# Optimization experiments

Hardware: AMD Instinct MI355X
Metric: run time of the kernel (lower is better)

Reference implementation:

```python
import jax, jax.numpy as jnp
import numpy as np

D_MODEL = 2048
N_HEADS = 8
EXPAND_K = 1
EXPAND_V = 2
DK = D_MODEL * EXPAND_K // N_HEADS      # 256 per-head key dim
DV = D_MODEL * EXPAND_V // N_HEADS      # 512 per-head value dim
INTER = 5632
EPS = 1e-6
CHUNK = 64


def setup_inputs() -> dict:
    key = jax.random.key(0)
    ks = jax.random.split(key, 12)
    d = D_MODEL
    s = lambda fan_in: 1.0 / np.sqrt(fan_in)
    return {
        "hidden_states": jax.random.normal(ks[0], (2, 2048, d), jnp.float32),
        "attn_norm_w": jnp.ones((d,), jnp.float32),
        "q_w": jax.random.normal(ks[1], (d, d * EXPAND_K), jnp.float32) * s(d),
        "k_w": jax.random.normal(ks[2], (d, d * EXPAND_K), jnp.float32) * s(d),
        "v_w": jax.random.normal(ks[3], (d, d * EXPAND_V), jnp.float32) * s(d),
        "g_w": jax.random.normal(ks[4], (d, d * EXPAND_V), jnp.float32) * s(d),
        "o_w": jax.random.normal(ks[5], (d * EXPAND_V, d), jnp.float32) * s(d * EXPAND_V),
        "gnorm_w": jnp.ones((DV,), jnp.float32),
        "mlp_norm_w": jnp.ones((d,), jnp.float32),
        "gate_w": jax.random.normal(ks[6], (d, INTER * 2), jnp.float32) * s(d),
        "down_w": jax.random.normal(ks[7], (INTER, d), jnp.float32) * s(INTER),
    }


def rmsnorm(x, w, eps=EPS):
    return x * jax.lax.rsqrt(jnp.mean(x * x, axis=-1, keepdims=True) + eps) * w


def rope(x):
    # x: [B, T, H, D]; non-interleaved rotary on full head dim
    T, D = x.shape[1], x.shape[-1]
    inv_freq = 1.0 / (10000.0 ** (jnp.arange(0, D, 2, dtype=jnp.float32) / D))
    ang = jnp.arange(T, dtype=jnp.float32)[:, None] * inv_freq  # [T, D/2]
    cos = jnp.cos(ang)[None, :, None, :]
    sin = jnp.sin(ang)[None, :, None, :]
    x1, x2 = jnp.split(x, 2, axis=-1)
    return jnp.concatenate([x1 * cos - x2 * sin, x2 * cos + x1 * sin], axis=-1)


def chunk_retention(q, k, v):
    # q,k: [B,T,H,Dk], v: [B,T,H,Dv]; chunkwise-recurrent RetNet retention
    B, T, H, Dk = q.shape
    Dv = v.shape[-1]
    C = CHUNK
    N = T // C
    gamma = 1.0 - jnp.exp2(-5.0 - jnp.arange(H, dtype=jnp.float32))  # [H]
    i = jnp.arange(C, dtype=jnp.float32)
    diff = i[:, None] - i[None, :]
    Dmask = jnp.where(diff >= 0, gamma[:, None, None] ** diff, 0.0)   # [H,C,C]
    cross_decay = gamma[:, None] ** (i[None, :] + 1.0)                # [H,C]
    k_decay = gamma[:, None] ** (C - 1.0 - i[None, :])                # [H,C]
    chunk_decay = gamma ** C                                          # [H]

    # -> [N, B, H, C, D]
    to_chunks = lambda x: jnp.moveaxis(
        x.reshape(B, N, C, H, x.shape[-1]).transpose(0, 1, 3, 2, 4), 1, 0)
    qc, kc, vc = to_chunks(q), to_chunks(k), to_chunks(v)

    def body(S, inp):
        qb, kb, vb = inp  # [B,H,C,Dk/Dv]
        attn = jnp.einsum('bhid,bhjd->bhij', qb, kb) * Dmask
        o_intra = jnp.einsum('bhij,bhje->bhie', attn, vb)
        o_cross = jnp.einsum('bhid,bhde->bhie', qb * cross_decay[None, :, :, None], S)
        S = chunk_decay[None, :, None, None] * S + \
            jnp.einsum('bhid,bhie->bhde', kb * k_decay[None, :, :, None], vb)
        return S, o_intra + o_cross

    S0 = jnp.zeros((B, H, Dk, Dv), q.dtype)
    _, o = jax.lax.scan(body, S0, (qc, kc, vc))  # o: [N,B,H,C,Dv]
    return jnp.moveaxis(o, 0, 1).transpose(0, 1, 3, 2, 4).reshape(B, T, H, Dv)


def reference(hidden_states, attn_norm_w, q_w, k_w, v_w, g_w, o_w, gnorm_w,
              mlp_norm_w, gate_w, down_w):
    B, T, d = hidden_states.shape
    residual = hidden_states
    h = rmsnorm(hidden_states, attn_norm_w)

    # MultiScaleRetention
    q = (h @ q_w).reshape(B, T, N_HEADS, DK)
    k = (h @ k_w).reshape(B, T, N_HEADS, DK)
    v = (h @ v_w).reshape(B, T, N_HEADS, DV)
    g = (h @ g_w).reshape(B, T, N_HEADS, DV)
    q, k = rope(q), rope(k)
    q = q * (DK ** -0.5)
    o = chunk_retention(q, k, v)
    # fused RMSNorm + swish gate (per head over Dv)
    o = rmsnorm(o, gnorm_w) * (g * jax.nn.sigmoid(g))
    h = o.reshape(B, T, N_HEADS * DV) @ o_w

    # fused-residual RMSNorm
    residual = h + residual
    h = rmsnorm(residual, mlp_norm_w)

    # SwiGLU MLP
    y = h @ gate_w
    gate, y = jnp.split(y, 2, axis=-1)
    h = (gate * jax.nn.sigmoid(gate) * y) @ down_w
    return residual + h
```

## Files before the change

### kernel.cpp

```cpp
#include <hip/hip_runtime.h>
#include <cstdint>
#include <cstddef>

typedef unsigned short u16;
typedef __attribute__((ext_vector_type(4))) float f32x4;
typedef __attribute__((ext_vector_type(4))) unsigned int u32x4;
typedef __attribute__((ext_vector_type(8))) short s16x8;

__device__ __forceinline__ float b2f(u16 u) {
  union { unsigned int i; float f; } x; x.i = ((unsigned int)u) << 16; return x.f;
}
__device__ __forceinline__ u16 f2b(float f) {
  union { float f; unsigned int i; } x; x.f = f;
  unsigned int i = x.i;
  i += 0x7fffu + ((i >> 16) & 1u);
  return (u16)(i >> 16);
}

__device__ __forceinline__ void mfma_bf16(f32x4& c, u32x4 a, u32x4 b) {
  union { u32x4 u; s16x8 s; } ua, ub;
  ua.u = a; ub.u = b;
  c = __builtin_amdgcn_mfma_f32_16x16x32_bf16(ua.s, ub.s, c, 0, 0, 0);
}

__device__ __forceinline__ void async_ld16(const u16* g, u16* l) {
  typedef __attribute__((address_space(1))) const unsigned int GU;
  typedef __attribute__((address_space(3))) unsigned int LU;
  __builtin_amdgcn_global_load_lds((GU*)g, (LU*)l, 16, 0, 0);
}

__global__ __launch_bounds__(256)
void transpose_cast_kernel(const float* __restrict__ in, u16* __restrict__ out,
                           int K, int N, int ldin) {
  __shared__ float tile[64][65];
  const int nb = N >> 6;
  const int bk = blockIdx.x / nb, bn = blockIdx.x % nb;
  const int k0 = bk * 64, n0 = bn * 64;
  const int tid = threadIdx.x;
#pragma unroll
  for (int p = 0; p < 16; ++p) {
    int idx = p * 256 + tid;
    int r = idx >> 6, c = idx & 63;
    tile[r][c] = in[(size_t)(k0 + r) * ldin + n0 + c];
  }
  __syncthreads();
#pragma unroll
  for (int p = 0; p < 16; ++p) {
    int idx = p * 256 + tid;
    int r = idx >> 6, c = idx & 63;
    out[(size_t)(n0 + r) * K + k0 + c] = f2b(tile[c][r]);
  }
}

__global__ __launch_bounds__(256)
void transpose_k_kernel(const u16* __restrict__ qk, u16* __restrict__ kt) {
  __shared__ u16 tile[64][72];
  const int bid = blockIdx.x;
  const int dd = bid & 3, tt = (bid >> 2) & 31;
  const int h = (bid >> 7) & 7, b = bid >> 10;
  const int t0 = tt * 64, d0 = dd * 64;
  const int tid = threadIdx.x;
#pragma unroll
  for (int p = 0; p < 2; ++p) {
    int idx = p * 256 + tid;
    int r = idx >> 3, cq = (idx & 7) * 8;
    *(uint4*)&tile[r][cq] =
        *(const uint4*)&qk[(size_t)(b * 2048 + t0 + r) * 4096 + 2048 + h * 256 + d0 + cq];
  }
  __syncthreads();
#pragma unroll
  for (int p = 0; p < 2; ++p) {
    int idx = p * 256 + tid;
    int r = idx >> 3, cq = (idx & 7) * 8;
    union { u16 h8[8]; uint4 v4; } o;
#pragma unroll
    for (int j = 0; j < 8; ++j) o.h8[j] = tile[cq + j][r];
    *(uint4*)&kt[((size_t)(b * 8 + h) * 256 + d0 + r) * 2048 + t0 + cq] = o.v4;
  }
}

__global__ __launch_bounds__(256)
void rmsnorm_cast_kernel(const float* __restrict__ x, const float* __restrict__ w,
                         u16* __restrict__ out) {
  const int row = blockIdx.x, tid = threadIdx.x;
  const float* xr = x + (size_t)row * 2048;
  float4 a = ((const float4*)xr)[tid * 2];
  float4 b = ((const float4*)xr)[tid * 2 + 1];
  float ss = a.x*a.x + a.y*a.y + a.z*a.z + a.w*a.w
           + b.x*b.x + b.y*b.y + b.z*b.z + b.w*b.w;
#pragma unroll
  for (int m = 32; m; m >>= 1) ss += __shfl_xor(ss, m);
  __shared__ float ps[4];
  if ((tid & 63) == 0) ps[tid >> 6] = ss;
  __syncthreads();
  const float sc = rsqrtf((ps[0] + ps[1] + ps[2] + ps[3]) * (1.0f / 2048.0f) + 1e-6f);
  const int base = tid * 8;
  const float vals[8] = {a.x, a.y, a.z, a.w, b.x, b.y, b.z, b.w};
  union { u16 h[8]; uint4 v4[2]; } o;
#pragma unroll
  for (int j = 0; j < 8; ++j) o.h[j] = f2b(vals[j] * sc * w[base + j]);
  *(uint4*)&out[(size_t)row * 2048 + base] = o.v4[0];
  *(uint4*)&out[(size_t)row * 2048 + base + 8] = o.v4[1];
}

__global__ __launch_bounds__(256)
void rmsnorm_bf16_kernel(const u16* __restrict__ x, const float* __restrict__ w,
                         u16* __restrict__ out) {
  const int row = blockIdx.x, tid = threadIdx.x;
  union { uint4 v4; u16 h[8]; } p;
  p.v4 = *(const uint4*)&x[(size_t)row * 2048 + tid * 8];
  float v[8];
  float ss = 0.f;
#pragma unroll
  for (int j = 0; j < 8; ++j) { v[j] = b2f(p.h[j]); ss += v[j] * v[j]; }
#pragma unroll
  for (int m = 32; m; m >>= 1) ss += __shfl_xor(ss, m);
  __shared__ float ps[4];
  if ((tid & 63) == 0) ps[tid >> 6] = ss;
  __syncthreads();
  const float sc = rsqrtf((ps[0] + ps[1] + ps[2] + ps[3]) * (1.0f / 2048.0f) + 1e-6f);
  union { u16 h[8]; uint4 v4; } o;
#pragma unroll
  for (int j = 0; j < 8; ++j) o.h[j] = f2b(v[j] * sc * w[tid * 8 + j]);
  *(uint4*)&out[(size_t)row * 2048 + tid * 8] = o.v4;
}

__global__ __launch_bounds__(256)
void rope_table_kernel(float* __restrict__ ct, float* __restrict__ st) {
  const int idx = blockIdx.x * 256 + threadIdx.x;
  const int t = idx >> 7, i = idx & 127;
  const float e = -(float)i * (0.0078125f * log2f(10000.0f));
  const float ang = (float)t * exp2f(e);
  ct[idx] = cosf(ang);
  st[idx] = sinf(ang);
}

__global__ __launch_bounds__(256)
void rope_apply_kernel(u16* __restrict__ x, const float* __restrict__ ct,
                       const float* __restrict__ st, int qoff, float scale) {
  const int gid = blockIdx.x * 256 + threadIdx.x;
  const int r = gid >> 8;
  const int rem = gid & 255;
  const int h = rem >> 5;
  const int i4 = (rem & 31) * 4;
  const int t = r & 2047;
  const size_t o1 = (size_t)r * 4096 + qoff + h * 256 + i4;
  union { ushort4 v; u16 h4[4]; } p1, p2, q1, q2;
  p1.v = *(ushort4*)&x[o1];
  p2.v = *(ushort4*)&x[o1 + 128];
  const float4 c = *(const float4*)&ct[t * 128 + i4];
  const float4 s = *(const float4*)&st[t * 128 + i4];
  const float cc[4] = {c.x, c.y, c.z, c.w};
  const float sn[4] = {s.x, s.y, s.z, s.w};
#pragma unroll
  for (int j = 0; j < 4; ++j) {
    float x1 = b2f(p1.h4[j]), x2 = b2f(p2.h4[j]);
    q1.h4[j] = f2b((x1 * cc[j] - x2 * sn[j]) * scale);
    q2.h4[j] = f2b((x2 * cc[j] + x1 * sn[j]) * scale);
  }
  *(ushort4*)&x[o1] = q1.v;
  *(ushort4*)&x[o1 + 128] = q2.v;
}

template <int BM, int EPI>
__global__ __launch_bounds__(512, 2)
void gemm4(const u16* __restrict__ A, const u16* __restrict__ Bt,
           void* Cout, const float* fsrc, const u16* hsrc,
           int N, int K, int lda, int pm, int pn, int gw) {
  constexpr int MF = BM / 32;
  constexpr int LA = BM / 128;
  constexpr int AH = BM * 64;
  constexpr int BH = 16384;
  constexpr int BUFB = 2 * AH + 2 * BH;
  constexpr int VMC = (BM == 256) ? 8 : 6;
  __shared__ __align__(16) char smem[2 * BUFB];

  const int tid = threadIdx.x;
  const int l = tid & 63, w = tid >> 6;
  const int lr = l & 15, hi = l >> 4;
  const int wm = w >> 2, wn = w & 3;
  const int xcd = blockIdx.x & 7;
  const int jj = blockIdx.x >> 3;
  const int gx = xcd % gw, gy = xcd / gw;
  const int bm = gx * pm + jj / pn;
  const int bn = gy * pn + jj % pn;
  const int nt = K >> 6;

  const int rA = tid >> 2;
  const int chx = (tid & 3) ^ ((tid >> 3) & 3);
  const u16* Ag = A + (size_t)(bm * BM + rA) * lda + chx * 8;
  const u16* Bg = Bt + (size_t)(bn * 256 + rA) * K + chx * 8;
  const int wb = w * 1024;

  int aoff[MF], boff[4];
#pragma unroll
  for (int mf = 0; mf < MF; ++mf) {
    int r = wm * (BM / 2) + mf * 16 + lr;
    aoff[mf] = (r * 4 + (hi ^ ((r >> 1) & 3))) * 16;
  }
#pragma unroll
  for (int nf = 0; nf < 4; ++nf) {
    int r = wn * 64 + nf * 16 + lr;
    boff[nf] = (r * 4 + (hi ^ ((r >> 1) & 3))) * 16;
  }

  f32x4 acc[MF][4];
#pragma unroll
  for (int m = 0; m < MF; ++m)
#pragma unroll
    for (int n = 0; n < 4; ++n) acc[m][n] = (f32x4){0.f, 0.f, 0.f, 0.f};
  u32x4 af[4], bf[4];

#define STA(kt, ks, bb)                                                        \
  { _Pragma("unroll") for (int t = 0; t < LA; ++t)                             \
      async_ld16(Ag + (size_t)t * 128 * lda + (kt) * 64 + (ks) * 32,           \
                 (u16*)(smem + (bb) * BUFB + (ks) * AH + t * 8192 + wb)); }
#define STB(kt, ks, bb)                                                        \
  { _Pragma("unroll") for (int t = 0; t < 2; ++t)                              \
      async_ld16(Bg + (size_t)t * 128 * K + (kt) * 64 + (ks) * 32,             \
                 (u16*)(smem + (bb) * BUFB + 2 * AH + (ks) * BH + t * 8192 + wb)); }
#define RDA(mh, ks, bb)                                                        \
  { _Pragma("unroll") for (int mf = 0; mf < 4; ++mf)                           \
      af[mf] = *(const u32x4*)(smem + (bb) * BUFB + (ks) * AH + aoff[(mh) * 4 + mf]); }
#define RDB(ks, bb)                                                            \
  { _Pragma("unroll") for (int nf = 0; nf < 4; ++nf)                           \
      bf[nf] = *(const u32x4*)(smem + (bb) * BUFB + 2 * AH + (ks) * BH + boff[nf]); }
#define MM(mh)                                                                 \
  { _Pragma("unroll") for (int mf = 0; mf < 4; ++mf)                           \
      _Pragma("unroll") for (int nf = 0; nf < 4; ++nf)                         \
        mfma_bf16(acc[(mh) * 4 + mf][nf], af[mf], bf[nf]); }
#define SB   __builtin_amdgcn_sched_barrier(0)
#define BARR __builtin_amdgcn_s_barrier()
#define VMW  asm volatile("s_waitcnt vmcnt(%0)" :: "n"(VMC) : "memory")

  STA(0, 0, 0); STB(0, 0, 0); STA(0, 1, 0); STB(0, 1, 0);
  STA(1, 0, 1); STB(1, 0, 1);
  SB; VMW; SB; BARR; SB;

  for (int i = 0; i < nt; ++i) {
    const int bb = i & 1, ob = bb ^ 1;
    const int t1 = (i + 1 < nt) ? i + 1 : 0;
    const int t2 = (i + 2 < nt) ? i + 2 : 0;
    if (BM == 256) {
      RDA(0, 0, bb); RDB(0, bb);
      STA(t1, 1, ob);
      SB; BARR;
      __builtin_amdgcn_s_setprio(1); MM(0); __builtin_amdgcn_s_setprio(0);
      SB; BARR; SB;
      RDA(1, 0, bb);
      STB(t1, 1, ob);
      SB; BARR;
      __builtin_amdgcn_s_setprio(1); MM(1); __builtin_amdgcn_s_setprio(0);
      SB; VMW; BARR; SB;
      RDA(0, 1, bb); RDB(1, bb);
      STA(t2, 0, bb);
      SB; BARR;
      __builtin_amdgcn_s_setprio(1); MM(0); __builtin_amdgcn_s_setprio(0);
      SB; BARR; SB;
      RDA(1, 1, bb);
      STB(t2, 0, bb);
      SB; BARR;
      __builtin_amdgcn_s_setprio(1); MM(1); __builtin_amdgcn_s_setprio(0);
      SB; VMW; BARR; SB;
    } else {
      RDA(0, 0, bb); RDB(0, bb);
      STA(t1, 1, ob); STB(t1, 1, ob);
      SB; BARR;
      __builtin_amdgcn_s_setprio(1); MM(0); __builtin_amdgcn_s_setprio(0);
      SB; VMW; BARR; SB;
      RDA(0, 1, bb); RDB(1, bb);
      STA(t2, 0, bb); STB(t2, 0, bb);
      SB; BARR;
      __builtin_amdgcn_s_setprio(1); MM(0); __builtin_amdgcn_s_setprio(0);
      SB; VMW; BARR; SB;
    }
  }
#undef STA
#undef STB
#undef RDA
#undef RDB
#undef MM
#undef SB
#undef BARR
#undef VMW

  const size_t crow0 = (size_t)(bm * BM + wm * (BM / 2));
  const int ccol0 = bn * 256 + wn * 64;
#pragma unroll
  for (int m = 0; m < MF; ++m)
#pragma unroll
    for (int n = 0; n < 4; ++n)
#pragma unroll
      for (int j2 = 0; j2 < 4; ++j2) {
        size_t r = crow0 + m * 16 + hi * 4 + j2;
        size_t c = (size_t)(ccol0 + n * 16 + lr);
        size_t idx = r * N + c;
        float a = acc[m][n][j2];
        if (EPI == 1) {
          ((u16*)Cout)[idx] = f2b(a);
        } else if (EPI == 2) {
          ((float*)Cout)[idx] = a + b2f(hsrc[idx]);
        } else if (EPI == 3) {
          float u = b2f(hsrc[idx]);
          ((u16*)Cout)[idx] = f2b(a / (1.0f + expf(-a)) * u);
        } else {
          ((u16*)Cout)[idx] = f2b(a + fsrc[idx]);
        }
      }
}

#define LGK 264
#define LGC 72
__global__ __launch_bounds__(512)
void retention_kernel(const u16* __restrict__ qk, const u16* __restrict__ kt,
                      const u16* __restrict__ v, u16* __restrict__ o) {
  __shared__ __align__(16) u16 ks[64 * LGK];
  __shared__ __align__(16) u16 stb[32 * LGK];
  __shared__ __align__(16) u16 ktd[256 * LGC];
  __shared__ __align__(16) u16 vts[32 * LGC];
  __shared__ __align__(16) u16 ab[64 * LGC];
  __shared__ float kdt[64];

  const int tid = threadIdx.x;
  const int l = tid & 63, w = tid >> 6;
  const int lr = l & 15, hi = l >> 4;
  const int wr = w >> 1;
  const int eb = w & 1;
  const int bid = blockIdx.x;
  const int g = bid & 15;
  const int sl = bid >> 4;
  const int hh = g & 7;
  const int b = g >> 3;
  const float gamma = 1.0f - exp2f(-5.0f - (float)hh);
  const float lg = log2f(gamma);
  const float cdk = exp2f(64.0f * lg);
  const int e0 = sl * 32;

  if (tid < 64) kdt[tid] = exp2f((float)(63 - tid) * lg);
  __syncthreads();

  f32x4 st[4];
#pragma unroll
  for (int t = 0; t < 4; ++t) st[t] = (f32x4){0.f, 0.f, 0.f, 0.f};

  for (int n = 0; n < 32; ++n) {
    const int row0 = b * 2048 + n * 64;
    const int t0 = n * 64;
#pragma unroll
    for (int t = 0; t < 4; ++t)
#pragma unroll
      for (int j = 0; j < 4; ++j)
        stb[(eb * 16 + hi * 4 + j) * LGK + (wr * 4 + t) * 16 + lr] = f2b(st[t][j]);
    u32x4 qf[8];
#pragma unroll
    for (int kk = 0; kk < 8; ++kk)
      qf[kk] = *(const u32x4*)&qk[(size_t)(row0 + wr * 16 + lr) * 4096 +
                                  hh * 256 + kk * 32 + hi * 8];
#pragma unroll
    for (int p = 0; p < 4; ++p) {
      int idx = p * 512 + tid;
      int c = idx >> 5, s = (idx & 31) * 8;
      *(uint4*)&ks[c * LGK + s] =
          *(const uint4*)&qk[(size_t)(row0 + c) * 4096 + 2048 + hh * 256 + s];
    }
#pragma unroll
    for (int p = 0; p < 4; ++p) {
      int idx = p * 512 + tid;
      int d = idx >> 3, cq = (idx & 7) * 8;
      union { uint4 v4; u16 h[8]; } pk;
      pk.v4 = *(const uint4*)&kt[((size_t)(b * 8 + hh) * 256 + d) * 2048 + t0 + cq];
      union { u16 h[8]; uint4 v4; } wo;
#pragma unroll
      for (int j2 = 0; j2 < 8; ++j2)
        wo.h[j2] = f2b(b2f(pk.h[j2]) * kdt[cq + j2]);
      *(uint4*)&ktd[d * LGC + cq] = wo.v4;
    }
#pragma unroll
    for (int p = 0; p < 4; ++p) {
      int c = (tid >> 5) + p * 16, e = tid & 31;
      vts[e * LGC + c] = v[(size_t)(row0 + c) * 4096 + hh * 512 + e0 + e];
    }
    __syncthreads();

    f32x4 att[2];
    att[0] = (f32x4){0.f, 0.f, 0.f, 0.f};
    att[1] = (f32x4){0.f, 0.f, 0.f, 0.f};
#pragma unroll
    for (int kk = 0; kk < 8; ++kk) {
#pragma unroll
      for (int jf = 0; jf < 2; ++jf) {
        u32x4 bb = *(const u32x4*)&ks[(eb * 32 + jf * 16 + lr) * LGK + kk * 32 + hi * 8];
        mfma_bf16(att[jf], qf[kk], bb);
      }
    }
#pragma unroll
    for (int jf = 0; jf < 2; ++jf)
#pragma unroll
      for (int j = 0; j < 4; ++j) {
        int i = wr * 16 + hi * 4 + j;
        int jc = eb * 32 + jf * 16 + lr;
        float mv = (i >= jc) ? exp2f((float)(i - jc) * lg) : 0.0f;
        ab[i * LGC + jc] = f2b(att[jf][j] * mv);
      }
    f32x4 occ = (f32x4){0.f, 0.f, 0.f, 0.f};
#pragma unroll
    for (int kk = 0; kk < 8; ++kk) {
      u32x4 bb = *(const u32x4*)&stb[(eb * 16 + lr) * LGK + kk * 32 + hi * 8];
      mfma_bf16(occ, qf[kk], bb);
    }
    __syncthreads();

#pragma unroll
    for (int j = 0; j < 4; ++j) {
      int i = wr * 16 + hi * 4 + j;
      occ[j] *= exp2f((float)(i + 1) * lg);
    }
#pragma unroll
    for (int kk = 0; kk < 2; ++kk) {
      u32x4 aa = *(const u32x4*)&ab[(wr * 16 + lr) * LGC + kk * 32 + hi * 8];
      u32x4 bb = *(const u32x4*)&vts[(eb * 16 + lr) * LGC + kk * 32 + hi * 8];
      mfma_bf16(occ, aa, bb);
    }
#pragma unroll
    for (int j = 0; j < 4; ++j) {
      int i = wr * 16 + hi * 4 + j;
      o[(size_t)(row0 + i) * 4096 + hh * 512 + e0 + eb * 16 + lr] = f2b(occ[j]);
    }
#pragma unroll
    for (int t = 0; t < 4; ++t) {
      st[t][0] *= cdk; st[t][1] *= cdk; st[t][2] *= cdk; st[t][3] *= cdk;
    }
#pragma unroll
    for (int kk = 0; kk < 2; ++kk) {
      u32x4 aa = *(const u32x4*)&vts[(eb * 16 + lr) * LGC + kk * 32 + hi * 8];
#pragma unroll
      for (int t = 0; t < 4; ++t) {
        u32x4 bb = *(const u32x4*)&ktd[((wr * 4 + t) * 16 + lr) * LGC + kk * 32 + hi * 8];
        mfma_bf16(st[t], aa, bb);
      }
    }
    __syncthreads();
  }
}

__global__ __launch_bounds__(64)
void gating_kernel(u16* __restrict__ o, const u16* __restrict__ g,
                   const float* __restrict__ gnw) {
  const int blk = blockIdx.x;
  const size_t base = (size_t)blk * 512;
  const int l = threadIdx.x;
  union { uint4 v4; u16 h[8]; } ov, gv;
  ov.v4 = *(const uint4*)&o[base + l * 8];
  float x[8];
  float ss = 0.f;
#pragma unroll
  for (int j = 0; j < 8; ++j) { x[j] = b2f(ov.h[j]); ss += x[j] * x[j]; }
#pragma unroll
  for (int m = 32; m; m >>= 1) ss += __shfl_xor(ss, m);
  const float sc = rsqrtf(ss * (1.0f / 512.0f) + 1e-6f);
  gv.v4 = *(const uint4*)&g[base + l * 8];
  union { u16 h[8]; uint4 v4; } ou;
#pragma unroll
  for (int j = 0; j < 8; ++j) {
    float gvf = b2f(gv.h[j]);
    float sig = 1.0f / (1.0f + expf(-gvf));
    ou.h[j] = f2b(x[j] * sc * gnw[l * 8 + j] * gvf * sig);
  }
  *(uint4*)&o[base + l * 8] = ou.v4;
}

extern "C" void kernel_launch(void* const* d_in, const int* in_sizes, int n_in,
                              void* d_out, int out_size, void* d_ws, size_t ws_size,
                              hipStream_t stream) {
  (void)in_sizes; (void)n_in; (void)out_size; (void)ws_size;
  const float* hidden      = (const float*)d_in[0];
  const float* attn_norm_w = (const float*)d_in[1];
  const float* q_w         = (const float*)d_in[2];
  const float* k_w         = (const float*)d_in[3];
  const float* v_w         = (const float*)d_in[4];
  const float* g_w         = (const float*)d_in[5];
  const float* o_w         = (const float*)d_in[6];
  const float* gnorm_w     = (const float*)d_in[7];
  const float* mlp_norm_w  = (const float*)d_in[8];
  const float* gate_w      = (const float*)d_in[9];
  const float* down_w      = (const float*)d_in[10];
  float* outp = (float*)d_out;

  char* ws = (char*)d_ws;
  size_t off = 0;
  auto alloc = [&](size_t bytes) -> char* {
    char* p = ws + off;
    off += (bytes + 255) & ~(size_t)255;
    return p;
  };
  u16*   W    = (u16*)alloc(23068672ULL);
  float* ctab = (float*)alloc(1048576ULL);
  float* stab = (float*)alloc(1048576ULL);
  u16*   hb   = (u16*)alloc(16777216ULL);
  u16*   qkb  = (u16*)alloc(33554432ULL);
  u16*   vb   = (u16*)alloc(33554432ULL);
  u16*   gb   = (u16*)alloc(33554432ULL);
  u16*   ob   = (u16*)alloc(33554432ULL);
  u16*   resb = (u16*)alloc(16777216ULL);
  u16*   ybU  = qkb;
  u16*   kt   = W;

  rope_table_kernel<<<1024, 256, 0, stream>>>(ctab, stab);
  rmsnorm_cast_kernel<<<4096, 256, 0, stream>>>(hidden, attn_norm_w, hb);

  transpose_cast_kernel<<<1024, 256, 0, stream>>>(q_w, W, 2048, 2048, 2048);
  transpose_cast_kernel<<<1024, 256, 0, stream>>>(k_w, W + 2048ULL * 2048, 2048, 2048, 2048);
  gemm4<256, 1><<<256, 512, 0, stream>>>(hb, W, (void*)qkb, nullptr, nullptr,
                                         4096, 2048, 2048, 8, 4, 2);
  transpose_cast_kernel<<<2048, 256, 0, stream>>>(v_w, W, 2048, 4096, 4096);
  gemm4<256, 1><<<256, 512, 0, stream>>>(hb, W, (void*)vb, nullptr, nullptr,
                                         4096, 2048, 2048, 8, 4, 2);
  transpose_cast_kernel<<<2048, 256, 0, stream>>>(g_w, W, 2048, 4096, 4096);
  gemm4<256, 1><<<256, 512, 0, stream>>>(hb, W, (void*)gb, nullptr, nullptr,
                                         4096, 2048, 2048, 8, 4, 2);

  rope_apply_kernel<<<4096, 256, 0, stream>>>(qkb, ctab, stab, 0, 0.0625f);
  rope_apply_kernel<<<4096, 256, 0, stream>>>(qkb, ctab, stab, 2048, 1.0f);
  transpose_k_kernel<<<2048, 256, 0, stream>>>(qkb, kt);

  retention_kernel<<<256, 512, 0, stream>>>(qkb, kt, vb, ob);

  gating_kernel<<<32768, 64, 0, stream>>>(ob, gb, gnorm_w);

  transpose_cast_kernel<<<2048, 256, 0, stream>>>(o_w, W, 4096, 2048, 2048);
  gemm4<128, 4><<<256, 512, 0, stream>>>(ob, W, (void*)resb, hidden, nullptr,
                                         2048, 4096, 4096, 16, 2, 2);

  rmsnorm_bf16_kernel<<<4096, 256, 0, stream>>>(resb, mlp_norm_w, hb);

  transpose_cast_kernel<<<2816, 256, 0, stream>>>(gate_w + 5632, W, 2048, 5632, 11264);
  gemm4<256, 1><<<352, 512, 0, stream>>>(hb, W, (void*)ybU, nullptr, nullptr,
                                         5632, 2048, 2048, 4, 11, 4);
  transpose_cast_kernel<<<2816, 256, 0, stream>>>(gate_w, W, 2048, 5632, 11264);
  gemm4<256, 3><<<352, 512, 0, stream>>>(hb, W, (void*)ybU, nullptr, ybU,
                                         5632, 2048, 2048, 4, 11, 4);

  transpose_cast_kernel<<<2816, 256, 0, stream>>>(down_w, W, 5632, 2048, 2048);
  gemm4<128, 2><<<256, 512, 0, stream>>>(ybU, W, (void*)outp, nullptr, resb,
                                         2048, 5632, 5632, 16, 2, 2);
}
```

Before: 920.1 us.

## Add simpler 256x256 K32 GEMM kernel and fuse V/G projections

Introduces a new gemm8 kernel with a 256x256 tile, K-step of 32, a single-stage async double buffer and one MFMA block per iteration. It replaces the BM=256 path of gemm4 for the QK, V/G and MLP gate GEMMs. The V and G weight matrices are now stored side by side so one GEMM with 512 blocks produces an interleaved [T, 8192] buffer, and the retention and gating kernels index it with the new stride. The aim is to cut pipeline-scheduling overhead and one launch, at the cost of a smaller K step per barrier and a larger workspace.

```diff
diff --git a/kernel.cpp b/kernel.cpp
--- a/kernel.cpp
+++ b/kernel.cpp
@@ -160,6 +160,111 @@
   }
   *(ushort4*)&x[o1] = q1.v;
   *(ushort4*)&x[o1 + 128] = q2.v;
+}
+
+template <int EPI>
+__global__ __launch_bounds__(512, 2)
+void gemm8(const u16* __restrict__ A, const u16* __restrict__ Bt,
+           void* Cout, const u16* hsrc, int N, int K, int lda,
+           int pm, int pn, int gw) {
+  __shared__ __align__(16) char smem[2][32768];
+  const int tid = threadIdx.x;
+  const int l = tid & 63, w = tid >> 6;
+  const int lr = l & 15, hi = l >> 4;
+  const int wm = w >> 2, wn = w & 3;
+  const int xcd = blockIdx.x & 7;
+  const int jj = blockIdx.x >> 3;
+  const int gx = xcd % gw, gy = xcd / gw;
+  const int bm = gx * pm + jj / pn;
+  const int bn = gy * pn + jj % pn;
+  const int nt = K >> 5;
+
+  const u16* Ap[2]; const u16* Bp[2];
+#pragma unroll
+  for (int t = 0; t < 2; ++t) {
+    int s = t * 512 + tid;
+    int row = s >> 2, ch = (s & 3) ^ ((s >> 3) & 3);
+    Ap[t] = A + (size_t)(bm * 256 + row) * lda + ch * 8;
+    Bp[t] = Bt + (size_t)(bn * 256 + row) * K + ch * 8;
+  }
+  const int dA0 = (0 * 512 + w * 64) * 16;
+  const int dA1 = (1 * 512 + w * 64) * 16;
+
+  int aoff[8], boff[4];
+#pragma unroll
+  for (int mf = 0; mf < 8; ++mf) {
+    int ra = wm * 128 + mf * 16 + lr;
+    aoff[mf] = (ra * 4 + (hi ^ ((ra >> 1) & 3))) * 16;
+  }
+#pragma unroll
+  for (int nf = 0; nf < 4; ++nf) {
+    int rb = wn * 64 + nf * 16 + lr;
+    boff[nf] = 16384 + (rb * 4 + (hi ^ ((rb >> 1) & 3))) * 16;
+  }
+
+  f32x4 acc[8][4];
+#pragma unroll
+  for (int m = 0; m < 8; ++m)
+#pragma unroll
+    for (int n = 0; n < 4; ++n) acc[m][n] = (f32x4){0.f, 0.f, 0.f, 0.f};
+
+#define SB __builtin_amdgcn_sched_barrier(0)
+  auto stage = [&](int i, int s) {
+    const int k0 = i * 32;
+    async_ld16(Ap[0] + k0, (u16*)(smem[s] + dA0));
+    async_ld16(Ap[1] + k0, (u16*)(smem[s] + dA1));
+    async_ld16(Bp[0] + k0, (u16*)(smem[s] + 16384 + dA0));
+    async_ld16(Bp[1] + k0, (u16*)(smem[s] + 16384 + dA1));
+  };
+
+  stage(0, 0);
+  SB;
+  for (int i = 0; i < nt; ++i) {
+    const int cur = i & 1;
+    const int ip = (i + 1 < nt) ? i + 1 : 0;
+    stage(ip, cur ^ 1);
+    SB;
+    asm volatile("s_waitcnt vmcnt(4)" ::: "memory");
+    SB;
+    __builtin_amdgcn_s_barrier();
+    SB;
+    const char* sm = smem[cur];
+    u32x4 af[8], bf[4];
+#pragma unroll
+    for (int f = 0; f < 8; ++f) af[f] = *(const u32x4*)(sm + aoff[f]);
+#pragma unroll
+    for (int f = 0; f < 4; ++f) bf[f] = *(const u32x4*)(sm + boff[f]);
+    __builtin_amdgcn_s_setprio(1);
+#pragma unroll
+    for (int m = 0; m < 8; ++m)
+#pragma unroll
+      for (int n = 0; n < 4; ++n) mfma_bf16(acc[m][n], af[m], bf[n]);
+    __builtin_amdgcn_s_setprio(0);
+    SB;
+    __builtin_amdgcn_s_barrier();
+    SB;
+  }
+#undef SB
+
+  const size_t crow0 = (size_t)(bm * 256 + wm * 128);
+  const int ccol0 = bn * 256 + wn * 64;
+#pragma unroll
+  for (int m = 0; m < 8; ++m)
+#pragma unroll
+    for (int n = 0; n < 4; ++n)
+#pragma unroll
+      for (int j2 = 0; j2 < 4; ++j2) {
+        size_t r = crow0 + m * 16 + hi * 4 + j2;
+        size_t c = (size_t)(ccol0 + n * 16 + lr);
+        size_t idx = r * N + c;
+        float a = acc[m][n][j2];
+        if (EPI == 1) {
+          ((u16*)Cout)[idx] = f2b(a);
+        } else {
+          float u = b2f(hsrc[idx]);
+          ((u16*)Cout)[idx] = f2b(a / (1.0f + expf(-a)) * u);
+        }
+      }
 }
 
 template <int BM, int EPI>
@@ -241,39 +346,16 @@
     const int bb = i & 1, ob = bb ^ 1;
     const int t1 = (i + 1 < nt) ? i + 1 : 0;
     const int t2 = (i + 2 < nt) ? i + 2 : 0;
-    if (BM == 256) {
-      RDA(0, 0, bb); RDB(0, bb);
-      STA(t1, 1, ob);
-      SB; BARR;
-      __builtin_amdgcn_s_setprio(1); MM(0); __builtin_amdgcn_s_setprio(0);
-      SB; BARR; SB;
-      RDA(1, 0, bb);
-      STB(t1, 1, ob);
-      SB; BARR;
-      __builtin_amdgcn_s_setprio(1); MM(1); __builtin_amdgcn_s_setprio(0);
-      SB; VMW; BARR; SB;
-      RDA(0, 1, bb); RDB(1, bb);
-      STA(t2, 0, bb);
-      SB; BARR;
-      __builtin_amdgcn_s_setprio(1); MM(0); __builtin_amdgcn_s_setprio(0);
-      SB; BARR; SB;
-      RDA(1, 1, bb);
-      STB(t2, 0, bb);
-      SB; BARR;
-      __builtin_amdgcn_s_setprio(1); MM(1); __builtin_amdgcn_s_setprio(0);
-      SB; VMW; BARR; SB;
-    } else {
-      RDA(0, 0, bb); RDB(0, bb);
-      STA(t1, 1, ob); STB(t1, 1, ob);
-      SB; BARR;
-      __builtin_amdgcn_s_setprio(1); MM(0); __builtin_amdgcn_s_setprio(0);
-      SB; VMW; BARR; SB;
-      RDA(0, 1, bb); RDB(1, bb);
-      STA(t2, 0, bb); STB(t2, 0, bb);
-      SB; BARR;
-      __builtin_amdgcn_s_setprio(1); MM(0); __builtin_amdgcn_s_setprio(0);
-      SB; VMW; BARR; SB;
-    }
+    RDA(0, 0, bb); RDB(0, bb);
+    STA(t1, 1, ob); STB(t1, 1, ob);
+    SB; BARR;
+    __builtin_amdgcn_s_setprio(1); MM(0); __builtin_amdgcn_s_setprio(0);
+    SB; VMW; BARR; SB;
+    RDA(0, 1, bb); RDB(1, bb);
+    STA(t2, 0, bb); STB(t2, 0, bb);
+    SB; BARR;
+    __builtin_amdgcn_s_setprio(1); MM(0); __builtin_amdgcn_s_setprio(0);
+    SB; VMW; BARR; SB;
   }
 #undef STA
 #undef STB
@@ -296,13 +378,8 @@
         size_t c = (size_t)(ccol0 + n * 16 + lr);
         size_t idx = r * N + c;
         float a = acc[m][n][j2];
-        if (EPI == 1) {
-          ((u16*)Cout)[idx] = f2b(a);
-        } else if (EPI == 2) {
+        if (EPI == 2) {
           ((float*)Cout)[idx] = a + b2f(hsrc[idx]);
-        } else if (EPI == 3) {
-          float u = b2f(hsrc[idx]);
-          ((u16*)Cout)[idx] = f2b(a / (1.0f + expf(-a)) * u);
         } else {
           ((u16*)Cout)[idx] = f2b(a + fsrc[idx]);
         }
@@ -378,7 +455,7 @@
 #pragma unroll
     for (int p = 0; p < 4; ++p) {
       int c = (tid >> 5) + p * 16, e = tid & 31;
-      vts[e * LGC + c] = v[(size_t)(row0 + c) * 4096 + hh * 512 + e0 + e];
+      vts[e * LGC + c] = v[(size_t)(row0 + c) * 8192 + hh * 512 + e0 + e];
     }
     __syncthreads();
 
@@ -447,10 +524,11 @@
 void gating_kernel(u16* __restrict__ o, const u16* __restrict__ g,
                    const float* __restrict__ gnw) {
   const int blk = blockIdx.x;
-  const size_t base = (size_t)blk * 512;
+  const size_t baseo = (size_t)blk * 512;
+  const size_t baseg = (size_t)(blk >> 3) * 8192 + (size_t)(blk & 7) * 512;
   const int l = threadIdx.x;
   union { uint4 v4; u16 h[8]; } ov, gv;
-  ov.v4 = *(const uint4*)&o[base + l * 8];
+  ov.v4 = *(const uint4*)&o[baseo + l * 8];
   float x[8];
   float ss = 0.f;
 #pragma unroll
@@ -458,7 +536,7 @@
 #pragma unroll
   for (int m = 32; m; m >>= 1) ss += __shfl_xor(ss, m);
   const float sc = rsqrtf(ss * (1.0f / 512.0f) + 1e-6f);
-  gv.v4 = *(const uint4*)&g[base + l * 8];
+  gv.v4 = *(const uint4*)&g[baseg + l * 8];
   union { u16 h[8]; uint4 v4; } ou;
 #pragma unroll
   for (int j = 0; j < 8; ++j) {
@@ -466,7 +544,7 @@
     float sig = 1.0f / (1.0f + expf(-gvf));
     ou.h[j] = f2b(x[j] * sc * gnw[l * 8 + j] * gvf * sig);
   }
-  *(uint4*)&o[base + l * 8] = ou.v4;
+  *(uint4*)&o[baseo + l * 8] = ou.v4;
 }
 
 extern "C" void kernel_launch(void* const* d_in, const int* in_sizes, int n_in,
@@ -493,13 +571,12 @@
     off += (bytes + 255) & ~(size_t)255;
     return p;
   };
-  u16*   W    = (u16*)alloc(23068672ULL);
+  u16*   W    = (u16*)alloc(33554432ULL);
   float* ctab = (float*)alloc(1048576ULL);
   float* stab = (float*)alloc(1048576ULL);
   u16*   hb   = (u16*)alloc(16777216ULL);
   u16*   qkb  = (u16*)alloc(33554432ULL);
-  u16*   vb   = (u16*)alloc(33554432ULL);
-  u16*   gb   = (u16*)alloc(33554432ULL);
+  u16*   vgb  = (u16*)alloc(67108864ULL);
   u16*   ob   = (u16*)alloc(33554432ULL);
   u16*   resb = (u16*)alloc(16777216ULL);
   u16*   ybU  = qkb;
@@ -510,22 +587,19 @@
 
   transpose_cast_kernel<<<1024, 256, 0, stream>>>(q_w, W, 2048, 2048, 2048);
   transpose_cast_kernel<<<1024, 256, 0, stream>>>(k_w, W + 2048ULL * 2048, 2048, 2048, 2048);
-  gemm4<256, 1><<<256, 512, 0, stream>>>(hb, W, (void*)qkb, nullptr, nullptr,
-                                         4096, 2048, 2048, 8, 4, 2);
+  gemm8<1><<<256, 512, 0, stream>>>(hb, W, (void*)qkb, nullptr, 4096, 2048, 2048, 8, 4, 2);
+
   transpose_cast_kernel<<<2048, 256, 0, stream>>>(v_w, W, 2048, 4096, 4096);
-  gemm4<256, 1><<<256, 512, 0, stream>>>(hb, W, (void*)vb, nullptr, nullptr,
-                                         4096, 2048, 2048, 8, 4, 2);
-  transpose_cast_kernel<<<2048, 256, 0, stream>>>(g_w, W, 2048, 4096, 4096);
-  gemm4<256, 1><<<256, 512, 0, stream>>>(hb, W, (void*)gb, nullptr, nullptr,
-                                         4096, 2048, 2048, 8, 4, 2);
+  transpose_cast_kernel<<<2048, 256, 0, stream>>>(g_w, W + 4096ULL * 2048, 2048, 4096, 4096);
+  gemm8<1><<<512, 512, 0, stream>>>(hb, W, (void*)vgb, nullptr, 8192, 2048, 2048, 8, 8, 2);
 
   rope_apply_kernel<<<4096, 256, 0, stream>>>(qkb, ctab, stab, 0, 0.0625f);
   rope_apply_kernel<<<4096, 256, 0, stream>>>(qkb, ctab, stab, 2048, 1.0f);
   transpose_k_kernel<<<2048, 256, 0, stream>>>(qkb, kt);
 
-  retention_kernel<<<256, 512, 0, stream>>>(qkb, kt, vb, ob);
-
-  gating_kernel<<<32768, 64, 0, stream>>>(ob, gb, gnorm_w);
+  retention_kernel<<<256, 512, 0, stream>>>(qkb, kt, vgb, ob);
+
+  gating_kernel<<<32768, 64, 0, stream>>>(ob, vgb + 4096, gnorm_w);
 
   transpose_cast_kernel<<<2048, 256, 0, stream>>>(o_w, W, 4096, 2048, 2048);
   gemm4<128, 4><<<256, 512, 0, stream>>>(ob, W, (void*)resb, hidden, nullptr,
@@ -534,11 +608,9 @@
   rmsnorm_bf16_kernel<<<4096, 256, 0, stream>>>(resb, mlp_norm_w, hb);
 
   transpose_cast_kernel<<<2816, 256, 0, stream>>>(gate_w + 5632, W, 2048, 5632, 11264);
-  gemm4<256, 1><<<352, 512, 0, stream>>>(hb, W, (void*)ybU, nullptr, nullptr,
-                                         5632, 2048, 2048, 4, 11, 4);
+  gemm8<1><<<352, 512, 0, stream>>>(hb, W, (void*)ybU, nullptr, 5632, 2048, 2048, 4, 11, 4);
   transpose_cast_kernel<<<2816, 256, 0, stream>>>(gate_w, W, 2048, 5632, 11264);
-  gemm4<256, 3><<<352, 512, 0, stream>>>(hb, W, (void*)ybU, nullptr, ybU,
-                                         5632, 2048, 2048, 4, 11, 4);
+  gemm8<3><<<352, 512, 0, stream>>>(hb, W, (void*)ybU, ybU, 5632, 2048, 2048, 4, 11, 4);
 
   transpose_cast_kernel<<<2816, 256, 0, stream>>>(down_w, W, 5632, 2048, 2048);
   gemm4<128, 2><<<256, 512, 0, stream>>>(ybU, W, (void*)outp, nullptr, resb,
```

Measured after the change: 955.3 us. +3.8%, slower.

## Add 128x128-tile double-buffered GEMM kernel for output and MLP projections

Applied to the files above, without the earlier changes.

Introduces gemm6, a 256-thread kernel with 128x128 output tiles and a K-step of 32. It double-buffers its shared-memory tiles, which are filled with async global-to-LDS loads using XOR-swizzled offsets. It replaces gemm4 for the output projection, both SwiGLU gate/up GEMMs and the down projection, launching many more, smaller blocks to improve occupancy and load balance. gemm4's epilogue is reduced to a plain bf16 store, since it is now only used for the QKV projections. The trade-off is less data reuse per tile and a barrier pair every 32-wide K step.

```diff
diff --git a/kernel.cpp b/kernel.cpp
--- a/kernel.cpp
+++ b/kernel.cpp
@@ -296,6 +296,102 @@
         size_t c = (size_t)(ccol0 + n * 16 + lr);
         size_t idx = r * N + c;
         float a = acc[m][n][j2];
+        (void)fsrc; (void)hsrc;
+        ((u16*)Cout)[idx] = f2b(a);
+      }
+}
+
+template <int EPI>
+__global__ __launch_bounds__(256, 4)
+void gemm6(const u16* __restrict__ A, const u16* __restrict__ Bt,
+           void* Cout, const float* fsrc, const u16* hsrc,
+           int N, int K, int lda) {
+  __shared__ __align__(16) char smem[2][16384];
+  const int tid = threadIdx.x;
+  const int l = tid & 63, w = tid >> 6;
+  const int lr = l & 15, hi = l >> 4;
+  const int wm = w >> 1, wn = w & 1;
+  const int cpx = (int)gridDim.x >> 3;
+  const int bid = (blockIdx.x & 7) * cpx + ((int)blockIdx.x >> 3);
+  const int nbn = N >> 7;
+  const int bm = bid / nbn, bn = bid % nbn;
+  const int nt = K >> 5;
+
+  const u16* Ap[2]; const u16* Bp[2];
+#pragma unroll
+  for (int t = 0; t < 2; ++t) {
+    int s = t * 256 + tid;
+    int row = s >> 2, ch = (s & 3) ^ ((s >> 3) & 3);
+    Ap[t] = A + (size_t)(bm * 128 + row) * lda + ch * 8;
+    Bp[t] = Bt + (size_t)(bn * 128 + row) * K + ch * 8;
+  }
+  const int dst0 = (0 * 256 + w * 64) * 16;
+  const int dst1 = (1 * 256 + w * 64) * 16;
+
+  int aoff[4], boff[4];
+#pragma unroll
+  for (int f = 0; f < 4; ++f) {
+    int ra = wm * 64 + f * 16 + lr;
+    aoff[f] = (ra * 4 + (hi ^ ((ra >> 1) & 3))) * 16;
+    int rb = wn * 64 + f * 16 + lr;
+    boff[f] = 8192 + (rb * 4 + (hi ^ ((rb >> 1) & 3))) * 16;
+  }
+
+  f32x4 acc[4][4];
+#pragma unroll
+  for (int m = 0; m < 4; ++m)
+#pragma unroll
+    for (int n = 0; n < 4; ++n) acc[m][n] = (f32x4){0.f, 0.f, 0.f, 0.f};
+
+#define SB __builtin_amdgcn_sched_barrier(0)
+  auto stage = [&](int i, int s) {
+    const int k0 = i * 32;
+    async_ld16(Ap[0] + k0, (u16*)(smem[s] + dst0));
+    async_ld16(Ap[1] + k0, (u16*)(smem[s] + dst1));
+    async_ld16(Bp[0] + k0, (u16*)(smem[s] + 8192 + dst0));
+    async_ld16(Bp[1] + k0, (u16*)(smem[s] + 8192 + dst1));
+  };
+
+  stage(0, 0);
+  SB;
+  for (int i = 0; i < nt; ++i) {
+    const int cur = i & 1;
+    const int ip = (i + 1 < nt) ? i + 1 : 0;
+    stage(ip, cur ^ 1);
+    SB;
+    asm volatile("s_waitcnt vmcnt(4)" ::: "memory");
+    SB;
+    __builtin_amdgcn_s_barrier();
+    SB;
+    u32x4 af[4], bf[4];
+#pragma unroll
+    for (int f = 0; f < 4; ++f) af[f] = *(const u32x4*)(smem[cur] + aoff[f]);
+#pragma unroll
+    for (int f = 0; f < 4; ++f) bf[f] = *(const u32x4*)(smem[cur] + boff[f]);
+    __builtin_amdgcn_s_setprio(1);
+#pragma unroll
+    for (int m = 0; m < 4; ++m)
+#pragma unroll
+      for (int n = 0; n < 4; ++n) mfma_bf16(acc[m][n], af[m], bf[n]);
+    __builtin_amdgcn_s_setprio(0);
+    SB;
+    __builtin_amdgcn_s_barrier();
+    SB;
+  }
+#undef SB
+
+  const size_t crow0 = (size_t)(bm * 128 + wm * 64);
+  const int ccol0 = bn * 128 + wn * 64;
+#pragma unroll
+  for (int m = 0; m < 4; ++m)
+#pragma unroll
+    for (int n = 0; n < 4; ++n)
+#pragma unroll
+      for (int j2 = 0; j2 < 4; ++j2) {
+        size_t r = crow0 + m * 16 + hi * 4 + j2;
+        size_t c = (size_t)(ccol0 + n * 16 + lr);
+        size_t idx = r * N + c;
+        float a = acc[m][n][j2];
         if (EPI == 1) {
           ((u16*)Cout)[idx] = f2b(a);
         } else if (EPI == 2) {
@@ -528,19 +624,15 @@
   gating_kernel<<<32768, 64, 0, stream>>>(ob, gb, gnorm_w);
 
   transpose_cast_kernel<<<2048, 256, 0, stream>>>(o_w, W, 4096, 2048, 2048);
-  gemm4<128, 4><<<256, 512, 0, stream>>>(ob, W, (void*)resb, hidden, nullptr,
-                                         2048, 4096, 4096, 16, 2, 2);
+  gemm6<4><<<512, 256, 0, stream>>>(ob, W, (void*)resb, hidden, nullptr, 2048, 4096, 4096);
 
   rmsnorm_bf16_kernel<<<4096, 256, 0, stream>>>(resb, mlp_norm_w, hb);
 
   transpose_cast_kernel<<<2816, 256, 0, stream>>>(gate_w + 5632, W, 2048, 5632, 11264);
-  gemm4<256, 1><<<352, 512, 0, stream>>>(hb, W, (void*)ybU, nullptr, nullptr,
-                                         5632, 2048, 2048, 4, 11, 4);
+  gemm6<1><<<1408, 256, 0, stream>>>(hb, W, (void*)ybU, nullptr, nullptr, 5632, 2048, 2048);
   transpose_cast_kernel<<<2816, 256, 0, stream>>>(gate_w, W, 2048, 5632, 11264);
-  gemm4<256, 3><<<352, 512, 0, stream>>>(hb, W, (void*)ybU, nullptr, ybU,
-                                         5632, 2048, 2048, 4, 11, 4);
+  gemm6<3><<<1408, 256, 0, stream>>>(hb, W, (void*)ybU, nullptr, ybU, 5632, 2048, 2048);
 
   transpose_cast_kernel<<<2816, 256, 0, stream>>>(down_w, W, 5632, 2048, 2048);
-  gemm4<128, 2><<<256, 512, 0, stream>>>(ybU, W, (void*)outp, nullptr, resb,
-                                         2048, 5632, 5632, 16, 2, 2);
-}
+  gemm6<2><<<512, 256, 0, stream>>>(ybU, W, (void*)outp, nullptr, resb, 2048, 5632, 5632);
+}
```

New measurement: 935.5 us. Within noise of the previous version (+1.7%).
